# Optimization experiments

Hardware: AMD Instinct MI355X
Metric: run time of the kernel (lower is better)

Reference implementation:

```python
import jax, jax.numpy as jnp
import numpy as np

BS, H, S, D = 2, 16, 4096, 64
BLOCK = 64
STRIDE_C = 3
NEG = -10000.0


def _global_index(seq_len, block_size, stride_c):
    # static Longformer-style global pattern: first token of each block plus
    # the last `stride_c` tokens of each block
    r = np.arange(seq_len)
    rem = r % block_size
    return np.nonzero((rem == 0) | (rem >= block_size - stride_c))[0]


def setup_inputs() -> dict:
    key = jax.random.key(0)
    k1, k2, k3 = jax.random.split(key, 3)
    q = jax.random.normal(k1, (BS, H, S, D), dtype=jnp.float32)
    k = jax.random.normal(k2, (BS, H, S, D), dtype=jnp.float32)
    v = jax.random.normal(k3, (BS, H, S, D), dtype=jnp.float32)
    mask = jnp.ones((BS, S), dtype=jnp.float32)  # all tokens valid -> pattern is static
    return {"query": q, "key": k, "value": v, "mask": mask}


def reference(query, key, value, mask):
    bs, h, S, d = query.shape
    block = BLOCK
    nb = S // block  # seq_len chosen as multiple of block_size, so pad_len == 0
    g_idx = jnp.asarray(_global_index(S, block, STRIDE_C))  # [G]

    # ---- block-local attention scores ----
    bq = query.reshape(bs, h, nb, block, d)
    bk = key.reshape(bs, h, nb, block, d)
    local = jnp.einsum('bhnxd,bhnyd->bhnxy', bq, bk)  # [bs,h,nb,block,block]
    # additive key-side mask (per key position within each block)
    key_mask = jnp.where(mask == 0.0, NEG, 0.0).reshape(bs, 1, nb, 1, block)
    local = (local + key_mask).reshape(bs, h, S, block)

    # ---- global-token attention scores ----
    gk = key[:, :, g_idx, :]    # [bs,h,G,d]
    gv = value[:, :, g_idx, :]  # [bs,h,G,d]
    gscores = jnp.einsum('bhsd,bhgd->bhsg', query, gk)  # [bs,h,S,G]
    gmask = jnp.where(mask[:, g_idx] == 0.0, NEG, 0.0)[:, None, None, :]
    gscores = gscores + gmask

    # ---- joint softmax over [local block | global tokens] ----
    scores = jnp.concatenate([local, gscores], axis=-1)  # [bs,h,S,block+G]
    probs = jax.nn.softmax(scores.astype(jnp.float32), axis=-1)

    # ---- weighted sums ----
    lp = probs[..., :block].reshape(bs, h, nb, block, block)
    bv = value.reshape(bs, h, nb, block, d)
    lout = jnp.matmul(lp, bv).reshape(bs, h, S, d)
    gout = jnp.einsum('bhsg,bhgd->bhsd', probs[..., block:], gv)
    return lout + gout
```

## Files before the change

kernel.cpp:

```cpp
#include <hip/hip_runtime.h>

#define NEGV -10000.0f

typedef _Float16 f16x8 __attribute__((ext_vector_type(8)));
typedef _Float16 f16x2 __attribute__((ext_vector_type(2)));
typedef float floatx4 __attribute__((ext_vector_type(4)));

__device__ __forceinline__ int src_row(int key, int nblk) {
    if (key < 64) return nblk * 64 + key;
    int g = key - 64;
    int p = g & 3;
    return (g >> 2) * 64 + (p ? (60 + p) : 0);
}

__global__ __launch_bounds__(256, 3)
void sparse_attn_kernel(const float* __restrict__ Q, const float* __restrict__ K,
                        const float* __restrict__ V, const float* __restrict__ M,
                        float* __restrict__ O)
{
    const int x    = blockIdx.x;
    const int bh   = (x & 7) * 4 + ((x >> 3) >> 6);
    const int nblk = (x >> 3) & 63;
    const int b    = bh >> 4;

    const size_t hoff = (size_t)bh * (4096 * 64);
    const float* Qh = Q + hoff;
    const float* Kh = K + hoff;
    const float* Vh = V + hoff;
    float*       Oh = O + hoff;
    const float* Mb = M + (size_t)b * 4096;

    __shared__ _Float16 smem[20480];

    const int tid  = threadIdx.x;
    const int lane = tid & 63;
    const int wv   = tid >> 6;
    const int m    = lane & 15;
    const int quad = lane >> 4;
    const int cg   = tid & 15;
    const int pg   = tid >> 4;

    float mv2[5];
    unsigned long long bb = 0ull;
    #pragma unroll
    for (int s = 0; s < 5; ++s) {
        float mval = Mb[src_row(s * 64 + lane, nblk)];
        bb |= __ballot(mval == 0.0f);
        mv2[s] = (mval == 0.0f) ? NEGV : 0.0f;
    }

    const int qrow = nblk * 64 + wv * 16 + m;
    f16x8 qf[2];
    #pragma unroll
    for (int c = 0; c < 2; ++c) {
        const float* src = Qh + (size_t)qrow * 64 + c * 32 + quad * 8;
        float4 f0 = *(const float4*)src;
        float4 f1 = *(const float4*)(src + 4);
        qf[c][0] = (_Float16)f0.x; qf[c][1] = (_Float16)f0.y;
        qf[c][2] = (_Float16)f0.z; qf[c][3] = (_Float16)f0.w;
        qf[c][4] = (_Float16)f1.x; qf[c][5] = (_Float16)f1.y;
        qf[c][6] = (_Float16)f1.z; qf[c][7] = (_Float16)f1.w;
    }

    #pragma unroll
    for (int it = 0; it < 10; ++it) {
        int S    = it * 256 + tid;
        int t    = S >> 7;
        int n    = S & 15;
        int col0 = ((S >> 6) & 1) * 32 + ((S & 63) >> 4) * 8;
        int lkey = 32 * (t >> 1) + 8 * (n >> 2) + 4 * (t & 1) + (n & 3);
        const float* src = Kh + (size_t)src_row(lkey, nblk) * 64 + col0;
        float4 f0 = *(const float4*)src;
        float4 f1 = *(const float4*)(src + 4);
        f16x8 o;
        o[0] = (_Float16)f0.x; o[1] = (_Float16)f0.y;
        o[2] = (_Float16)f0.z; o[3] = (_Float16)f0.w;
        o[4] = (_Float16)f1.x; o[5] = (_Float16)f1.y;
        o[6] = (_Float16)f1.z; o[7] = (_Float16)f1.w;
        *(f16x8*)(&smem[S * 8]) = o;
    }

    float4 v0a[5], v0b[5];
    #pragma unroll
    for (int it = 0; it < 5; ++it) {
        int l0 = 2 * (it * 16 + pg);
        v0a[it] = *(const float4*)(Vh + (size_t)src_row(l0,     nblk) * 64 + cg * 4);
        v0b[it] = *(const float4*)(Vh + (size_t)src_row(l0 + 1, nblk) * 64 + cg * 4);
    }

    __syncthreads();

    floatx4 acc[20] = {};
    #pragma unroll
    for (int t = 0; t < 20; ++t) {
        #pragma unroll
        for (int c = 0; c < 2; ++c) {
            f16x8 kf = *(const f16x8*)(&smem[(t * 2 + c) * 512 + lane * 8]);
            acc[t] = __builtin_amdgcn_mfma_f32_16x16x32_f16(kf, qf[c], acc[t], 0, 0, 0);
        }
    }

    __syncthreads();

    auto vt_store = [&](int l0, const float4& f0, const float4& f1) {
        int kc2   = l0 >> 5;
        int q2    = (l0 & 31) >> 3;
        int j0    = l0 & 7;
        int td    = cg >> 2;
        int sw    = td << 4;
        int lbase = (kc2 * 4 + td) * 512 + q2 * 128 + (cg & 3) * 32 + j0;
        f16x2 pk0; pk0[0] = (_Float16)f0.x; pk0[1] = (_Float16)f1.x;
        *(f16x2*)(&smem[(lbase +  0) ^ sw]) = pk0;
        f16x2 pk1; pk1[0] = (_Float16)f0.y; pk1[1] = (_Float16)f1.y;
        *(f16x2*)(&smem[(lbase +  8) ^ sw]) = pk1;
        f16x2 pk2; pk2[0] = (_Float16)f0.z; pk2[1] = (_Float16)f1.z;
        *(f16x2*)(&smem[(lbase + 16) ^ sw]) = pk2;
        f16x2 pk3; pk3[0] = (_Float16)f0.w; pk3[1] = (_Float16)f1.w;
        *(f16x2*)(&smem[(lbase + 24) ^ sw]) = pk3;
    };

    #pragma unroll
    for (int it = 0; it < 5; ++it)
        vt_store(2 * (it * 16 + pg), v0a[it], v0b[it]);

    float4 v1a[5], v1b[5];
    #pragma unroll
    for (int it = 0; it < 5; ++it) {
        int l0 = 2 * ((5 + it) * 16 + pg);
        v1a[it] = *(const float4*)(Vh + (size_t)src_row(l0,     nblk) * 64 + cg * 4);
        v1b[it] = *(const float4*)(Vh + (size_t)src_row(l0 + 1, nblk) * 64 + cg * 4);
    }

    if (bb != 0ull) {
        #pragma unroll
        for (int t = 0; t < 20; ++t) {
            int lb = 32 * ((t >> 1) & 1) + 4 * (t & 1) + 8 * quad;
            #pragma unroll
            for (int r = 0; r < 4; ++r)
                acc[t][r] += __shfl(mv2[t >> 2], lb + r, 64);
        }
    }

    float rmax = -3e38f;
    #pragma unroll
    for (int t = 0; t < 20; ++t)
        #pragma unroll
        for (int r = 0; r < 4; ++r)
            rmax = fmaxf(rmax, acc[t][r]);
    rmax = fmaxf(rmax, __shfl_xor(rmax, 16, 64));
    rmax = fmaxf(rmax, __shfl_xor(rmax, 32, 64));
    float rsum = 0.f;
    #pragma unroll
    for (int t = 0; t < 20; ++t)
        #pragma unroll
        for (int r = 0; r < 4; ++r) {
            float e = __expf(acc[t][r] - rmax);
            acc[t][r] = e;
            rsum += e;
        }
    rsum += __shfl_xor(rsum, 16, 64);
    rsum += __shfl_xor(rsum, 32, 64);
    float rinv = 1.0f / rsum;

    #pragma unroll
    for (int it = 0; it < 5; ++it)
        vt_store(2 * ((5 + it) * 16 + pg), v1a[it], v1b[it]);

    f16x8 pf[10];
    #pragma unroll
    for (int k2 = 0; k2 < 10; ++k2) {
        #pragma unroll
        for (int r = 0; r < 4; ++r) {
            pf[k2][r]     = (_Float16)acc[2 * k2][r];
            pf[k2][4 + r] = (_Float16)acc[2 * k2 + 1][r];
        }
    }

    __syncthreads();

    floatx4 oacc[4] = {};
    #pragma unroll
    for (int k2 = 0; k2 < 10; ++k2) {
        #pragma unroll
        for (int t = 0; t < 4; ++t) {
            f16x8 vf = *(const f16x8*)(&smem[(k2 * 4 + t) * 512 + ((lane * 8) ^ (t << 4))]);
            oacc[t] = __builtin_amdgcn_mfma_f32_16x16x32_f16(pf[k2], vf, oacc[t], 0, 0, 0);
        }
    }

    float rinvr[4];
    #pragma unroll
    for (int r = 0; r < 4; ++r)
        rinvr[r] = __shfl(rinv, quad * 4 + r, 64);
    #pragma unroll
    for (int t = 0; t < 4; ++t)
        #pragma unroll
        for (int r = 0; r < 4; ++r)
            Oh[(size_t)(nblk * 64 + wv * 16 + quad * 4 + r) * 64 + t * 16 + m] =
                oacc[t][r] * rinvr[r];
}

extern "C" void kernel_launch(void* const* d_in, const int* in_sizes, int n_in,
                              void* d_out, int out_size, void* d_ws, size_t ws_size,
                              hipStream_t stream) {
    const float* q    = (const float*)d_in[0];
    const float* k    = (const float*)d_in[1];
    const float* v    = (const float*)d_in[2];
    const float* mask = (const float*)d_in[3];
    float* out = (float*)d_out;
    (void)in_sizes; (void)n_in; (void)out_size; (void)d_ws; (void)ws_size;
    sparse_attn_kernel<<<2 * 16 * 64, 256, 0, stream>>>(q, k, v, mask, out);
}
```

Baseline: 156.8 us.

## Process four query blocks per workgroup, reusing staged global K/V in LDS

Each workgroup now handles four consecutive 64-row query blocks instead of one. The 256 global-token K/V rows are converted to fp16 and staged in shared memory once and reused across all four blocks, which removes redundant global loads and conversions. The next block's local Q/K/V are prefetched into registers while the current block computes. In exchange the grid drops to 512 workgroups, shared memory doubles, launch bounds fall to 2 waves per SIMD, and probabilities are normalized before the PV matmul.

```diff
diff --git a/kernel.cpp b/kernel.cpp
--- a/kernel.cpp
+++ b/kernel.cpp
@@ -13,15 +13,25 @@
     return (g >> 2) * 64 + (p ? (60 + p) : 0);
 }
 
-__global__ __launch_bounds__(256, 3)
+__device__ __forceinline__ f16x8 cvt8(const float4& f0, const float4& f1) {
+    f16x8 o;
+    o[0] = (_Float16)f0.x; o[1] = (_Float16)f0.y;
+    o[2] = (_Float16)f0.z; o[3] = (_Float16)f0.w;
+    o[4] = (_Float16)f1.x; o[5] = (_Float16)f1.y;
+    o[6] = (_Float16)f1.z; o[7] = (_Float16)f1.w;
+    return o;
+}
+
+__global__ __launch_bounds__(256, 2)
 void sparse_attn_kernel(const float* __restrict__ Q, const float* __restrict__ K,
                         const float* __restrict__ V, const float* __restrict__ M,
                         float* __restrict__ O)
 {
-    const int x    = blockIdx.x;
-    const int bh   = (x & 7) * 4 + ((x >> 3) >> 6);
-    const int nblk = (x >> 3) & 63;
-    const int b    = bh >> 4;
+    const int x     = blockIdx.x;
+    const int bh    = (x & 7) * 4 + ((x >> 3) >> 4);
+    const int slice = (x >> 3) & 15;
+    const int b     = bh >> 4;
+    const int nblk0 = slice * 4;
 
     const size_t hoff = (size_t)bh * (4096 * 64);
     const float* Qh = Q + hoff;
@@ -30,7 +40,8 @@
     float*       Oh = O + hoff;
     const float* Mb = M + (size_t)b * 4096;
 
-    __shared__ _Float16 smem[20480];
+    __shared__ _Float16 smem[40960];
+    constexpr int GVT = 16384, LKo = 32768, LVT = 36864;
 
     const int tid  = threadIdx.x;
     const int lane = tid & 63;
@@ -40,75 +51,11 @@
     const int cg   = tid & 15;
     const int pg   = tid >> 4;
 
-    float mv2[5];
-    unsigned long long bb = 0ull;
-    #pragma unroll
-    for (int s = 0; s < 5; ++s) {
-        float mval = Mb[src_row(s * 64 + lane, nblk)];
-        bb |= __ballot(mval == 0.0f);
-        mv2[s] = (mval == 0.0f) ? NEGV : 0.0f;
-    }
-
-    const int qrow = nblk * 64 + wv * 16 + m;
-    f16x8 qf[2];
-    #pragma unroll
-    for (int c = 0; c < 2; ++c) {
-        const float* src = Qh + (size_t)qrow * 64 + c * 32 + quad * 8;
-        float4 f0 = *(const float4*)src;
-        float4 f1 = *(const float4*)(src + 4);
-        qf[c][0] = (_Float16)f0.x; qf[c][1] = (_Float16)f0.y;
-        qf[c][2] = (_Float16)f0.z; qf[c][3] = (_Float16)f0.w;
-        qf[c][4] = (_Float16)f1.x; qf[c][5] = (_Float16)f1.y;
-        qf[c][6] = (_Float16)f1.z; qf[c][7] = (_Float16)f1.w;
-    }
-
-    #pragma unroll
-    for (int it = 0; it < 10; ++it) {
-        int S    = it * 256 + tid;
-        int t    = S >> 7;
-        int n    = S & 15;
-        int col0 = ((S >> 6) & 1) * 32 + ((S & 63) >> 4) * 8;
-        int lkey = 32 * (t >> 1) + 8 * (n >> 2) + 4 * (t & 1) + (n & 3);
-        const float* src = Kh + (size_t)src_row(lkey, nblk) * 64 + col0;
-        float4 f0 = *(const float4*)src;
-        float4 f1 = *(const float4*)(src + 4);
-        f16x8 o;
-        o[0] = (_Float16)f0.x; o[1] = (_Float16)f0.y;
-        o[2] = (_Float16)f0.z; o[3] = (_Float16)f0.w;
-        o[4] = (_Float16)f1.x; o[5] = (_Float16)f1.y;
-        o[6] = (_Float16)f1.z; o[7] = (_Float16)f1.w;
-        *(f16x8*)(&smem[S * 8]) = o;
-    }
-
-    float4 v0a[5], v0b[5];
-    #pragma unroll
-    for (int it = 0; it < 5; ++it) {
-        int l0 = 2 * (it * 16 + pg);
-        v0a[it] = *(const float4*)(Vh + (size_t)src_row(l0,     nblk) * 64 + cg * 4);
-        v0b[it] = *(const float4*)(Vh + (size_t)src_row(l0 + 1, nblk) * 64 + cg * 4);
-    }
-
-    __syncthreads();
-
-    floatx4 acc[20] = {};
-    #pragma unroll
-    for (int t = 0; t < 20; ++t) {
-        #pragma unroll
-        for (int c = 0; c < 2; ++c) {
-            f16x8 kf = *(const f16x8*)(&smem[(t * 2 + c) * 512 + lane * 8]);
-            acc[t] = __builtin_amdgcn_mfma_f32_16x16x32_f16(kf, qf[c], acc[t], 0, 0, 0);
-        }
-    }
-
-    __syncthreads();
-
-    auto vt_store = [&](int l0, const float4& f0, const float4& f1) {
-        int kc2   = l0 >> 5;
-        int q2    = (l0 & 31) >> 3;
-        int j0    = l0 & 7;
+    auto vt_store_at = [&](int base, int k2, const float4& f0, const float4& f1) {
         int td    = cg >> 2;
         int sw    = td << 4;
-        int lbase = (kc2 * 4 + td) * 512 + q2 * 128 + (cg & 3) * 32 + j0;
+        int lbase = base + (k2 * 4 + td) * 512 + (pg >> 2) * 128
+                  + (cg & 3) * 32 + 2 * (pg & 3);
         f16x2 pk0; pk0[0] = (_Float16)f0.x; pk0[1] = (_Float16)f1.x;
         *(f16x2*)(&smem[(lbase +  0) ^ sw]) = pk0;
         f16x2 pk1; pk1[0] = (_Float16)f0.y; pk1[1] = (_Float16)f1.y;
@@ -118,86 +65,173 @@
         f16x2 pk3; pk3[0] = (_Float16)f0.w; pk3[1] = (_Float16)f1.w;
         *(f16x2*)(&smem[(lbase + 24) ^ sw]) = pk3;
     };
-
-    #pragma unroll
-    for (int it = 0; it < 5; ++it)
-        vt_store(2 * (it * 16 + pg), v0a[it], v0b[it]);
-
-    float4 v1a[5], v1b[5];
-    #pragma unroll
-    for (int it = 0; it < 5; ++it) {
-        int l0 = 2 * ((5 + it) * 16 + pg);
-        v1a[it] = *(const float4*)(Vh + (size_t)src_row(l0,     nblk) * 64 + cg * 4);
-        v1b[it] = *(const float4*)(Vh + (size_t)src_row(l0 + 1, nblk) * 64 + cg * 4);
-    }
-
-    if (bb != 0ull) {
+    auto q_load = [&](int nblk, float4* qn) {
+        const float* src = Qh + (size_t)(nblk * 64 + wv * 16 + m) * 64 + quad * 8;
+        qn[0] = *(const float4*)src;        qn[1] = *(const float4*)(src + 4);
+        qn[2] = *(const float4*)(src + 32); qn[3] = *(const float4*)(src + 36);
+    };
+    auto lk_load = [&](int nblk, float4* kn) {
+        #pragma unroll
+        for (int s2 = 0; s2 < 2; ++s2) {
+            int S    = s2 * 256 + tid;
+            int t    = S >> 7;
+            int n    = S & 15;
+            int col0 = ((S >> 6) & 1) * 32 + ((S & 63) >> 4) * 8;
+            int lkey = 32 * (t >> 1) + 8 * (n >> 2) + 4 * (t & 1) + (n & 3);
+            const float* src = Kh + (size_t)(nblk * 64 + lkey) * 64 + col0;
+            kn[2 * s2]     = *(const float4*)src;
+            kn[2 * s2 + 1] = *(const float4*)(src + 4);
+        }
+    };
+    auto lk_write = [&](const float4* kn) {
+        #pragma unroll
+        for (int s2 = 0; s2 < 2; ++s2) {
+            int S = s2 * 256 + tid;
+            *(f16x8*)(&smem[LKo + S * 8]) = cvt8(kn[2 * s2], kn[2 * s2 + 1]);
+        }
+    };
+    auto lv_load = [&](int nblk, float4* vn) {
+        #pragma unroll
+        for (int g = 0; g < 2; ++g) {
+            int l0 = 2 * (g * 16 + pg);
+            vn[2 * g]     = *(const float4*)(Vh + (size_t)(nblk * 64 + l0) * 64 + cg * 4);
+            vn[2 * g + 1] = *(const float4*)(Vh + (size_t)(nblk * 64 + l0 + 1) * 64 + cg * 4);
+        }
+    };
+    auto lv_write = [&](const float4* vn) {
+        vt_store_at(LVT, 0, vn[0], vn[1]);
+        vt_store_at(LVT, 1, vn[2], vn[3]);
+    };
+
+    float mv2[5];
+    unsigned long long bbg = 0ull;
+    #pragma unroll
+    for (int s = 1; s < 5; ++s) {
+        float mval = Mb[src_row(s * 64 + lane, 0)];
+        bbg |= __ballot(mval == 0.0f);
+        mv2[s] = (mval == 0.0f) ? NEGV : 0.0f;
+    }
+
+    #pragma unroll
+    for (int it = 0; it < 8; ++it) {
+        int S    = it * 256 + tid;
+        int t    = (S >> 7) + 4;
+        int n    = S & 15;
+        int col0 = ((S >> 6) & 1) * 32 + ((S & 63) >> 4) * 8;
+        int lkey = 32 * (t >> 1) + 8 * (n >> 2) + 4 * (t & 1) + (n & 3);
+        const float* src = Kh + (size_t)src_row(lkey, 0) * 64 + col0;
+        float4 f0 = *(const float4*)src;
+        float4 f1 = *(const float4*)(src + 4);
+        *(f16x8*)(&smem[S * 8]) = cvt8(f0, f1);
+    }
+    #pragma unroll
+    for (int it = 2; it < 10; ++it) {
+        int l0 = 2 * (it * 16 + pg);
+        float4 f0 = *(const float4*)(Vh + (size_t)src_row(l0,     0) * 64 + cg * 4);
+        float4 f1 = *(const float4*)(Vh + (size_t)src_row(l0 + 1, 0) * 64 + cg * 4);
+        vt_store_at(GVT, it - 2, f0, f1);
+    }
+    float4 qn[4], kn[4], vn[4];
+    q_load(nblk0, qn);
+    lk_load(nblk0, kn);
+    lv_load(nblk0, vn);
+    lk_write(kn);
+    lv_write(vn);
+    float mloc = Mb[(size_t)nblk0 * 64 + lane];
+
+    __syncthreads();
+
+    #pragma unroll
+    for (int i = 0; i < 4; ++i) {
+        const int nblk = nblk0 + i;
+        f16x8 qf[2] = { cvt8(qn[0], qn[1]), cvt8(qn[2], qn[3]) };
+        const float mloc_c = mloc;
+
+        floatx4 acc[20];
         #pragma unroll
         for (int t = 0; t < 20; ++t) {
-            int lb = 32 * ((t >> 1) & 1) + 4 * (t & 1) + 8 * quad;
+            acc[t] = floatx4{0.f, 0.f, 0.f, 0.f};
+            #pragma unroll
+            for (int c = 0; c < 2; ++c) {
+                const int slab = (t < 4) ? (LKo + (t * 2 + c) * 512)
+                                         : (((t - 4) * 2 + c) * 512);
+                f16x8 kf = *(const f16x8*)(&smem[slab + lane * 8]);
+                acc[t] = __builtin_amdgcn_mfma_f32_16x16x32_f16(kf, qf[c], acc[t], 0, 0, 0);
+            }
+        }
+
+        if (i < 3) {
+            q_load(nblk + 1, qn);
+            lk_load(nblk + 1, kn);
+            lv_load(nblk + 1, vn);
+            mloc = Mb[(size_t)(nblk + 1) * 64 + lane];
+        }
+
+        unsigned long long bb = bbg | __ballot(mloc_c == 0.0f);
+        if (bb != 0ull) {
+            mv2[0] = (mloc_c == 0.0f) ? NEGV : 0.0f;
+            #pragma unroll
+            for (int t = 0; t < 20; ++t) {
+                int lb = 32 * ((t >> 1) & 1) + 4 * (t & 1) + 8 * quad;
+                #pragma unroll
+                for (int r = 0; r < 4; ++r)
+                    acc[t][r] += __shfl(mv2[t >> 2], lb + r, 64);
+            }
+        }
+
+        float rmax = -3e38f;
+        #pragma unroll
+        for (int t = 0; t < 20; ++t)
             #pragma unroll
             for (int r = 0; r < 4; ++r)
-                acc[t][r] += __shfl(mv2[t >> 2], lb + r, 64);
-        }
-    }
-
-    float rmax = -3e38f;
-    #pragma unroll
-    for (int t = 0; t < 20; ++t)
-        #pragma unroll
-        for (int r = 0; r < 4; ++r)
-            rmax = fmaxf(rmax, acc[t][r]);
-    rmax = fmaxf(rmax, __shfl_xor(rmax, 16, 64));
-    rmax = fmaxf(rmax, __shfl_xor(rmax, 32, 64));
-    float rsum = 0.f;
-    #pragma unroll
-    for (int t = 0; t < 20; ++t)
-        #pragma unroll
-        for (int r = 0; r < 4; ++r) {
-            float e = __expf(acc[t][r] - rmax);
-            acc[t][r] = e;
-            rsum += e;
-        }
-    rsum += __shfl_xor(rsum, 16, 64);
-    rsum += __shfl_xor(rsum, 32, 64);
-    float rinv = 1.0f / rsum;
-
-    #pragma unroll
-    for (int it = 0; it < 5; ++it)
-        vt_store(2 * ((5 + it) * 16 + pg), v1a[it], v1b[it]);
-
-    f16x8 pf[10];
-    #pragma unroll
-    for (int k2 = 0; k2 < 10; ++k2) {
-        #pragma unroll
-        for (int r = 0; r < 4; ++r) {
-            pf[k2][r]     = (_Float16)acc[2 * k2][r];
-            pf[k2][4 + r] = (_Float16)acc[2 * k2 + 1][r];
-        }
-    }
-
-    __syncthreads();
-
-    floatx4 oacc[4] = {};
-    #pragma unroll
-    for (int k2 = 0; k2 < 10; ++k2) {
-        #pragma unroll
-        for (int t = 0; t < 4; ++t) {
-            f16x8 vf = *(const f16x8*)(&smem[(k2 * 4 + t) * 512 + ((lane * 8) ^ (t << 4))]);
-            oacc[t] = __builtin_amdgcn_mfma_f32_16x16x32_f16(pf[k2], vf, oacc[t], 0, 0, 0);
-        }
-    }
-
-    float rinvr[4];
-    #pragma unroll
-    for (int r = 0; r < 4; ++r)
-        rinvr[r] = __shfl(rinv, quad * 4 + r, 64);
-    #pragma unroll
-    for (int t = 0; t < 4; ++t)
-        #pragma unroll
-        for (int r = 0; r < 4; ++r)
-            Oh[(size_t)(nblk * 64 + wv * 16 + quad * 4 + r) * 64 + t * 16 + m] =
-                oacc[t][r] * rinvr[r];
+                rmax = fmaxf(rmax, acc[t][r]);
+        rmax = fmaxf(rmax, __shfl_xor(rmax, 16, 64));
+        rmax = fmaxf(rmax, __shfl_xor(rmax, 32, 64));
+        float rsum = 0.f;
+        #pragma unroll
+        for (int t = 0; t < 20; ++t)
+            #pragma unroll
+            for (int r = 0; r < 4; ++r) {
+                float e = __expf(acc[t][r] - rmax);
+                acc[t][r] = e;
+                rsum += e;
+            }
+        rsum += __shfl_xor(rsum, 16, 64);
+        rsum += __shfl_xor(rsum, 32, 64);
+        const float rinv = 1.0f / rsum;
+
+        floatx4 oacc[4] = {};
+        #pragma unroll
+        for (int k2 = 0; k2 < 10; ++k2) {
+            f16x8 p;
+            #pragma unroll
+            for (int r = 0; r < 4; ++r) {
+                p[r]     = (_Float16)(acc[2 * k2][r]     * rinv);
+                p[4 + r] = (_Float16)(acc[2 * k2 + 1][r] * rinv);
+            }
+            #pragma unroll
+            for (int t = 0; t < 4; ++t) {
+                const int base = (k2 < 2) ? (LVT + (k2 * 4 + t) * 512)
+                                          : (GVT + ((k2 - 2) * 4 + t) * 512);
+                f16x8 vf = *(const f16x8*)(&smem[base + ((lane * 8) ^ (t << 4))]);
+                oacc[t] = __builtin_amdgcn_mfma_f32_16x16x32_f16(p, vf, oacc[t], 0, 0, 0);
+            }
+        }
+
+        #pragma unroll
+        for (int t = 0; t < 4; ++t)
+            #pragma unroll
+            for (int r = 0; r < 4; ++r)
+                Oh[(size_t)(nblk * 64 + wv * 16 + quad * 4 + r) * 64 + t * 16 + m] =
+                    oacc[t][r];
+
+        if (i < 3) {
+            __syncthreads();
+            lk_write(kn);
+            lv_write(vn);
+            __syncthreads();
+        }
+    }
 }
 
 extern "C" void kernel_launch(void* const* d_in, const int* in_sizes, int n_in,
@@ -209,5 +243,5 @@
     const float* mask = (const float*)d_in[3];
     float* out = (float*)d_out;
     (void)in_sizes; (void)n_in; (void)out_size; (void)d_ws; (void)ws_size;
-    sparse_attn_kernel<<<2 * 16 * 64, 256, 0, stream>>>(q, k, v, mask, out);
-}
+    sparse_attn_kernel<<<512, 256, 0, stream>>>(q, k, v, mask, out);
+}
```

Result: faster. 145.3 us (-7.3%).
